# Optimization experiments

Measured on AMD Instinct MI355X. Metric: run time of the kernel, lower is better.

## Reference

```python
import jax, jax.numpy as jnp
import numpy as np

K = 3
PAD = 1
FS = 64  # feature_size == img_size for k=3, pad=1, stride=1
BN_EPS = 1e-5


def _unfold(x):
    # x: (B, C, H, W) -> (B, C*K*K, FS*FS), torch.nn.Unfold ordering (C-major, then kh, kw)
    B, C, H, W = x.shape
    xp = jnp.pad(x, ((0, 0), (0, 0), (PAD, PAD), (PAD, PAD)))
    patches = jnp.stack(
        [xp[:, :, i:i + FS, j:j + FS] for i in range(K) for j in range(K)],
        axis=2,
    )  # (B, C, K*K, FS, FS)
    return patches.reshape(B, C * K * K, FS * FS)


def setup_inputs() -> dict:
    key = jax.random.key(0)
    k1, k2, k3, k4, k5 = jax.random.split(key, 5)
    B, C, O = 32, 8, 32
    P = C * K * K  # 72
    return {
        "x": jax.random.normal(k1, (B, C, FS, FS), dtype=jnp.float32),
        "weight": jax.random.normal(k2, (1, O, P, FS * FS), dtype=jnp.float32) * 0.05,
        "bias": jax.random.normal(k3, (1, O, FS * FS), dtype=jnp.float32) * 0.05,
        "gamma": jax.random.uniform(k4, (O,), dtype=jnp.float32, minval=0.5, maxval=1.5),
        "beta": jax.random.normal(k5, (O,), dtype=jnp.float32) * 0.1,
    }


def reference(x, weight, bias, gamma, beta):
    B = x.shape[0]
    patches = _unfold(x)  # (B, P, F2)
    # per-pixel weights: (O, P, F2) contracted with patches over P
    y = jnp.einsum('opf,bpf->bof', weight[0], patches)  # (B, O, F2)
    y = y + bias  # (1, O, F2) broadcasts
    y = y.reshape(B, -1, FS, FS)
    # BatchNorm2d, training mode (biased batch variance)
    mean = jnp.mean(y, axis=(0, 2, 3), keepdims=True)
    var = jnp.mean(jnp.square(y - mean), axis=(0, 2, 3), keepdims=True)
    y = (y - mean) * jax.lax.rsqrt(var + BN_EPS)
    y = y * gamma[None, :, None, None] + beta[None, :, None, None]
    return y
```

## Files before the change

kernel.cpp:

```cpp
#include <hip/hip_runtime.h>

#define Oo    32
#define F2    4096
#define GRID  256
#define SLOTS 64
#define NTOT  (32 * F2)

typedef _Float16 h2 __attribute__((ext_vector_type(2)));
typedef _Float16 h8 __attribute__((ext_vector_type(8)));

#if __has_builtin(__builtin_amdgcn_fdot2)
#define DOT2(a, b, c) __builtin_amdgcn_fdot2((a), (b), (c), false)
#else
__device__ __forceinline__ float DOT2(h2 a, h2 b, float c) {
    return c + (float)a.x * (float)b.x + (float)a.y * (float)b.y;
}
#endif

__device__ __forceinline__ unsigned pkh2f(float a, float b) {
    h2 t; t.x = (_Float16)a; t.y = (_Float16)b;
    return __builtin_bit_cast(unsigned, t);
}
__device__ __forceinline__ h2 bch2(unsigned u) { return __builtin_bit_cast(h2, u); }

template <typename YT>
__global__ __launch_bounds__(512) void svconv_kernel(
    const float* __restrict__ x, const float* __restrict__ wgt,
    const float* __restrict__ bias, YT* __restrict__ y,
    float* __restrict__ psum, float* __restrict__ psumsq)
{
    __shared__ __align__(16) unsigned ldsX[3 * 32 * 68];
    __shared__ __align__(16) unsigned ldsW[2 * 9 * 8 * 64];

    const int tid = threadIdx.x;
    const int f   = tid & 63;
    const int bq  = tid >> 6;
    const int oq  = blockIdx.x >> 6;
    const int h   = blockIdx.x & 63;
    const int col = h * 64 + f;

    const bool wOK = (tid < 288);
    int wg = 0, wl = 0;
    {
        int s = wOK ? tid : 0;
        int o_ = s / 36, rm = s - 36 * o_;
        int k_ = rm >> 2, q_ = rm & 3;
        wg = ((oq * 8 + o_) * 72 + k_) * F2 + h * 64 + 16 * q_;
        wl = (k_ * 8 + o_) * 64 + 16 * q_;
    }

    bool xOK = false;
    int xg = 0, xl = 0;
    {
        int s = (tid < 384) ? tid : 0;
        int kh_ = s >> 7, b_ = (s >> 2) & 31, q_ = s & 3;
        int gh = h - 1 + kh_;
        xOK = (tid < 384) && ((unsigned)gh < 64u);
        xg = b_ * 32768 + gh * 64 + 16 * q_;
        xl = (kh_ * 32 + b_) * 68 + 16 * q_;
    }

    const int wi0 = (f == 0)  ? 64 : f - 1;
    const int wi2 = (f == 63) ? 65 : f + 1;

    float bz[8];
#pragma unroll
    for (int j = 0; j < 8; ++j) bz[j] = bias[(oq * 8 + j) * F2 + col];

    float acc[8][4];
#pragma unroll
    for (int j = 0; j < 8; ++j)
#pragma unroll
        for (int i = 0; i < 4; ++i) acc[j][i] = 0.f;

    float4 xr0[4], xr1[4], wr0[4], wr1[4];

    auto ISSUEX = [&](int cp) {
        if (xOK) {
            const int c0 = xg + cp * 8192;
#pragma unroll
            for (int e = 0; e < 4; ++e) {
                xr0[e] = *(const float4*)(x + c0 + 4 * e);
                xr1[e] = *(const float4*)(x + c0 + 4096 + 4 * e);
            }
        }
    };
    auto ISSUEW = [&](int cp) {
        if (wOK) {
            const int g0 = wg + cp * 18 * F2;
#pragma unroll
            for (int e = 0; e < 4; ++e) {
                wr0[e] = *(const float4*)(wgt + g0 + 4 * e);
                wr1[e] = *(const float4*)(wgt + g0 + 9 * F2 + 4 * e);
            }
        }
    };
    auto WRITEX = [&]() {
        if (xOK) {
#pragma unroll
            for (int e = 0; e < 4; ++e) {
                uint4 pk;
                pk.x = pkh2f(xr0[e].x, xr1[e].x);
                pk.y = pkh2f(xr0[e].y, xr1[e].y);
                pk.z = pkh2f(xr0[e].z, xr1[e].z);
                pk.w = pkh2f(xr0[e].w, xr1[e].w);
                *(uint4*)&ldsX[xl + 4 * e] = pk;
            }
        }
    };
    auto WRITEW = [&](int buf) {
        if (wOK) {
#pragma unroll
            for (int e = 0; e < 4; ++e) {
                uint4 pk;
                pk.x = pkh2f(wr0[e].x, wr1[e].x);
                pk.y = pkh2f(wr0[e].y, wr1[e].y);
                pk.z = pkh2f(wr0[e].z, wr1[e].z);
                pk.w = pkh2f(wr0[e].w, wr1[e].w);
                *(uint4*)&ldsW[buf * 4608 + wl + 4 * e] = pk;
            }
        }
    };
    auto COMPUTE = [&](int wbuf) {
        const unsigned* wb = &ldsW[wbuf * 4608];
#pragma unroll
        for (int k = 0; k < 9; ++k) {
            const int kh = k / 3, kw = k - 3 * kh;
            const int wi = (kw == 0) ? wi0 : ((kw == 1) ? f : wi2);
            h2 wv[8];
#pragma unroll
            for (int j = 0; j < 8; ++j) wv[j] = bch2(wb[k * 512 + j * 64 + f]);
#pragma unroll
            for (int i = 0; i < 4; ++i) {
                h2 xv = bch2(ldsX[(kh * 32 + bq * 4 + i) * 68 + wi]);
#pragma unroll
                for (int j = 0; j < 8; ++j)
                    acc[j][i] = DOT2(wv[j], xv, acc[j][i]);
            }
        }
    };

    ISSUEX(0); ISSUEW(0);
    for (int i = tid; i < 3 * 32 * 68; i += 512) ldsX[i] = 0u;
    __syncthreads();
    WRITEX(); WRITEW(0);
    ISSUEX(1); ISSUEW(1);
    __syncthreads();

#pragma unroll
    for (int cp = 0; cp < 4; ++cp) {
        COMPUTE(cp & 1);
        if (cp < 3) {
            __syncthreads();
            WRITEX(); WRITEW((cp + 1) & 1);
            if (cp < 2) { ISSUEX(cp + 2); ISSUEW(cp + 2); }
            __syncthreads();
        }
    }
    __syncthreads();

    float s_[8], ss_[8];
#pragma unroll
    for (int j = 0; j < 8; ++j) {
        s_[j] = 0.f; ss_[j] = 0.f;
#pragma unroll
        for (int i = 0; i < 4; ++i) {
            float a = acc[j][i] + bz[j];
            y[(size_t)((bq * 4 + i) * Oo + oq * 8 + j) * F2 + col] = (YT)a;
            s_[j] += a; ss_[j] = fmaf(a, a, ss_[j]);
        }
    }
    if (psum != nullptr) {
#pragma unroll
        for (int j = 0; j < 8; ++j)
#pragma unroll
            for (int d = 32; d >= 1; d >>= 1) {
                s_[j]  += __shfl_down(s_[j],  d, 64);
                ss_[j] += __shfl_down(ss_[j], d, 64);
            }
        float* scr = (float*)ldsX;
        if (f == 0) {
#pragma unroll
            for (int j = 0; j < 8; ++j) {
                scr[bq * 8 + j]      = s_[j];
                scr[64 + bq * 8 + j] = ss_[j];
            }
        }
        __syncthreads();
        if (tid < 64) {
            int j = tid >> 3, g = tid & 7;
            float v  = scr[g * 8 + j];
            float vv = scr[64 + g * 8 + j];
#pragma unroll
            for (int d = 4; d >= 1; d >>= 1) {
                v  += __shfl_down(v,  d, 8);
                vv += __shfl_down(vv, d, 8);
            }
            if (g == 0) {
                psum[(oq * 8 + j) * SLOTS + h]   = v;
                psumsq[(oq * 8 + j) * SLOTS + h] = vv;
            }
        }
    }
}

__global__ __launch_bounds__(64) void bnstats_kernel(
    const float* __restrict__ psum, const float* __restrict__ psumsq,
    const float* __restrict__ gamma, const float* __restrict__ beta,
    float* __restrict__ scsh)
{
    const int o = blockIdx.x;
    const int t = threadIdx.x;
    float s  = psum[o * SLOTS + t];
    float ss = psumsq[o * SLOTS + t];
#pragma unroll
    for (int d = 32; d >= 1; d >>= 1) {
        s  += __shfl_down(s, d, 64);
        ss += __shfl_down(ss, d, 64);
    }
    if (t == 0) {
        float mean = s / (float)NTOT;
        float var  = ss / (float)NTOT - mean * mean;
        float rstd = rsqrtf(var + 1e-5f);
        float scl  = gamma[o] * rstd;
        scsh[o]      = scl;
        scsh[Oo + o] = beta[o] - mean * scl;
    }
}

__global__ __launch_bounds__(256) void bnapply_f16_kernel(
    const _Float16* __restrict__ yh, const float* __restrict__ scsh,
    float* __restrict__ y)
{
    int i = blockIdx.x * 256 + threadIdx.x;
    h8 v = ((const h8*)yh)[i];
    int o = (i >> 9) & 31;
    float scl = scsh[o], sh = scsh[Oo + o];
    float4 lo, hi;
    lo.x = fmaf((float)v[0], scl, sh);
    lo.y = fmaf((float)v[1], scl, sh);
    lo.z = fmaf((float)v[2], scl, sh);
    lo.w = fmaf((float)v[3], scl, sh);
    hi.x = fmaf((float)v[4], scl, sh);
    hi.y = fmaf((float)v[5], scl, sh);
    hi.z = fmaf((float)v[6], scl, sh);
    hi.w = fmaf((float)v[7], scl, sh);
    ((float4*)y)[2 * i]     = lo;
    ((float4*)y)[2 * i + 1] = hi;
}

__global__ __launch_bounds__(256) void bnapply_kernel(
    float* __restrict__ y, const float* __restrict__ scsh)
{
    int i = blockIdx.x * 256 + threadIdx.x;
    float4 v = ((const float4*)y)[i];
    int o = (i >> 10) & 31;
    float scl = scsh[o], sh = scsh[Oo + o];
    v.x = fmaf(v.x, scl, sh);
    v.y = fmaf(v.y, scl, sh);
    v.z = fmaf(v.z, scl, sh);
    v.w = fmaf(v.w, scl, sh);
    ((float4*)y)[i] = v;
}

__global__ __launch_bounds__(256) void bnreduce_y_kernel(
    const float* __restrict__ y, float* __restrict__ seg, float* __restrict__ segsq)
{
    const int o  = blockIdx.x >> 3;
    const int sg = blockIdx.x & 7;
    const int t  = threadIdx.x;
    float s = 0.f, ss = 0.f;
    for (int i = t; i < 4 * 1024; i += 256) {
        int b   = sg * 4 + (i >> 10);
        int fof = (i & 1023) * 4;
        float4 v = *(const float4*)(y + (size_t)(b * Oo + o) * F2 + fof);
        s  += (v.x + v.y) + (v.z + v.w);
        ss += v.x * v.x + v.y * v.y + v.z * v.z + v.w * v.w;
    }
#pragma unroll
    for (int d = 32; d >= 1; d >>= 1) {
        s  += __shfl_down(s, d, 64);
        ss += __shfl_down(ss, d, 64);
    }
    __shared__ float ls[4], lss[4];
    int wv = t >> 6, ln = t & 63;
    if (ln == 0) { ls[wv] = s; lss[wv] = ss; }
    __syncthreads();
    if (t == 0) {
        seg[blockIdx.x]   = (ls[0] + ls[1]) + (ls[2] + ls[3]);
        segsq[blockIdx.x] = (lss[0] + lss[1]) + (lss[2] + lss[3]);
    }
}

__global__ __launch_bounds__(256) void bnstats2_kernel(
    const float* __restrict__ seg, const float* __restrict__ segsq,
    const float* __restrict__ gamma, const float* __restrict__ beta,
    float* __restrict__ scsh)
{
    const int t = threadIdx.x;
    const int o = t >> 3, g = t & 7;
    float v  = seg[t];
    float vv = segsq[t];
#pragma unroll
    for (int d = 4; d >= 1; d >>= 1) {
        v  += __shfl_down(v,  d, 8);
        vv += __shfl_down(vv, d, 8);
    }
    if (g == 0) {
        float mean = v / (float)NTOT;
        float var  = vv / (float)NTOT - mean * mean;
        float rstd = rsqrtf(var + 1e-5f);
        float scl  = gamma[o] * rstd;
        scsh[o]      = scl;
        scsh[Oo + o] = beta[o] - mean * scl;
    }
}

extern "C" void kernel_launch(void* const* d_in, const int* in_sizes, int n_in,
                              void* d_out, int out_size, void* d_ws, size_t ws_size,
                              hipStream_t stream)
{
    const float* x     = (const float*)d_in[0];
    const float* wgt   = (const float*)d_in[1];
    const float* bias  = (const float*)d_in[2];
    const float* gamma = (const float*)d_in[3];
    const float* beta  = (const float*)d_in[4];
    float* y = (float*)d_out;

    const size_t n_elems    = (size_t)NTOT * Oo;
    const size_t yh_bytes   = n_elems * sizeof(_Float16);
    const size_t psum_bytes = (size_t)(2 * Oo * SLOTS + 2 * Oo) * sizeof(float);

    if (ws_size >= yh_bytes + psum_bytes) {
        _Float16* yh  = (_Float16*)d_ws;
        float* psum   = (float*)((char*)d_ws + yh_bytes);
        float* psumsq = psum + Oo * SLOTS;
        float* scsh   = psumsq + Oo * SLOTS;
        svconv_kernel<_Float16><<<GRID, 512, 0, stream>>>(x, wgt, bias, yh, psum, psumsq);
        bnstats_kernel<<<Oo, 64, 0, stream>>>(psum, psumsq, gamma, beta, scsh);
        bnapply_f16_kernel<<<(int)(n_elems / 8 / 256), 256, 0, stream>>>(yh, scsh, y);
    } else if (ws_size >= psum_bytes) {
        float* psum   = (float*)d_ws;
        float* psumsq = psum + Oo * SLOTS;
        float* scsh   = psumsq + Oo * SLOTS;
        svconv_kernel<float><<<GRID, 512, 0, stream>>>(x, wgt, bias, y, psum, psumsq);
        bnstats_kernel<<<Oo, 64, 0, stream>>>(psum, psumsq, gamma, beta, scsh);
        bnapply_kernel<<<(int)(n_elems / 4 / 256), 256, 0, stream>>>(y, scsh);
    } else {
        float* seg   = (float*)d_ws;
        float* segsq = seg + 256;
        float* scsh  = segsq + 256;
        svconv_kernel<float><<<GRID, 512, 0, stream>>>(x, wgt, bias, y, nullptr, nullptr);
        bnreduce_y_kernel<<<256, 256, 0, stream>>>(y, seg, segsq);
        bnstats2_kernel<<<1, 256, 0, stream>>>(seg, segsq, gamma, beta, scsh);
        bnapply_kernel<<<(int)(n_elems / 4 / 256), 256, 0, stream>>>(y, scsh);
    }
}
```

Baseline: 32.06 us.

## Transpose LDS layouts for vector reads and double-buffer X with one barrier

Weights and inputs are stored in LDS in transposed, padded layouts: per-pixel weights are packed so the 8 output channels sit contiguously, and input is stored pixel-major with batch contiguous and halo columns. This lets COMPUTE fetch its operands with a few 128-bit LDS reads instead of many scalar reads per tap. X is now double-buffered like W, so each pipeline step writes the next buffer before computing the current one and needs one barrier instead of two. The trade-offs are scattered 32-bit LDS stores when writing X, strided global weight loads, and a larger LDS footprint.

```diff
diff --git a/kernel.cpp b/kernel.cpp
--- a/kernel.cpp
+++ b/kernel.cpp
@@ -5,6 +5,8 @@
 #define GRID  256
 #define SLOTS 64
 #define NTOT  (32 * F2)
+#define WBUF  6912
+#define XBUF  7128
 
 typedef _Float16 h2 __attribute__((ext_vector_type(2)));
 typedef _Float16 h8 __attribute__((ext_vector_type(8)));
@@ -29,8 +31,8 @@
     const float* __restrict__ bias, YT* __restrict__ y,
     float* __restrict__ psum, float* __restrict__ psumsq)
 {
-    __shared__ __align__(16) unsigned ldsX[3 * 32 * 68];
-    __shared__ __align__(16) unsigned ldsW[2 * 9 * 8 * 64];
+    __shared__ __align__(16) unsigned ldsW[2 * WBUF];
+    __shared__ __align__(16) unsigned ldsX[2 * XBUF];
 
     const int tid = threadIdx.x;
     const int f   = tid & 63;
@@ -43,25 +45,22 @@
     int wg = 0, wl = 0;
     {
         int s = wOK ? tid : 0;
-        int o_ = s / 36, rm = s - 36 * o_;
-        int k_ = rm >> 2, q_ = rm & 3;
-        wg = ((oq * 8 + o_) * 72 + k_) * F2 + h * 64 + 16 * q_;
-        wl = (k_ * 8 + o_) * 64 + 16 * q_;
+        int o4 = s / 144, rm = s - 144 * o4;
+        int k_ = rm >> 4, q_ = rm & 15;
+        wg = ((oq * 8 + o4 * 4) * 72 + k_) * F2 + h * 64 + 4 * q_;
+        wl = (k_ * 64 + 4 * q_) * 12 + o4 * 4;
     }
 
     bool xOK = false;
-    int xg = 0, xl = 0;
+    int xg = 0, xkh = 0, xq = 0, xb_ = 0;
     {
         int s = (tid < 384) ? tid : 0;
-        int kh_ = s >> 7, b_ = (s >> 2) & 31, q_ = s & 3;
-        int gh = h - 1 + kh_;
+        xkh = s >> 7; int r = s & 127;
+        xq = r >> 5; xb_ = r & 31;
+        int gh = h - 1 + xkh;
         xOK = (tid < 384) && ((unsigned)gh < 64u);
-        xg = b_ * 32768 + gh * 64 + 16 * q_;
-        xl = (kh_ * 32 + b_) * 68 + 16 * q_;
-    }
-
-    const int wi0 = (f == 0)  ? 64 : f - 1;
-    const int wi2 = (f == 63) ? 65 : f + 1;
+        xg = xb_ * 32768 + gh * 64 + 16 * xq;
+    }
 
     float bz[8];
 #pragma unroll
@@ -73,7 +72,7 @@
 #pragma unroll
         for (int i = 0; i < 4; ++i) acc[j][i] = 0.f;
 
-    float4 xr0[4], xr1[4], wr0[4], wr1[4];
+    float4 xr0[4], xr1[4], wA[4], wB[4];
 
     auto ISSUEX = [&](int cp) {
         if (xOK) {
@@ -89,75 +88,73 @@
         if (wOK) {
             const int g0 = wg + cp * 18 * F2;
 #pragma unroll
+            for (int j = 0; j < 4; ++j) {
+                wA[j] = *(const float4*)(wgt + g0 + j * 72 * F2);
+                wB[j] = *(const float4*)(wgt + g0 + j * 72 * F2 + 9 * F2);
+            }
+        }
+    };
+    auto WRITEX = [&](int buf) {
+        if (xOK) {
+            unsigned* xd = ldsX + buf * XBUF + xkh * (66 * 36) + xb_;
+#pragma unroll
             for (int e = 0; e < 4; ++e) {
-                wr0[e] = *(const float4*)(wgt + g0 + 4 * e);
-                wr1[e] = *(const float4*)(wgt + g0 + 9 * F2 + 4 * e);
-            }
-        }
-    };
-    auto WRITEX = [&]() {
-        if (xOK) {
-#pragma unroll
-            for (int e = 0; e < 4; ++e) {
-                uint4 pk;
-                pk.x = pkh2f(xr0[e].x, xr1[e].x);
-                pk.y = pkh2f(xr0[e].y, xr1[e].y);
-                pk.z = pkh2f(xr0[e].z, xr1[e].z);
-                pk.w = pkh2f(xr0[e].w, xr1[e].w);
-                *(uint4*)&ldsX[xl + 4 * e] = pk;
+                const float* a = (const float*)&xr0[e];
+                const float* b = (const float*)&xr1[e];
+#pragma unroll
+                for (int i = 0; i < 4; ++i)
+                    xd[(16 * xq + 4 * e + i + 1) * 36] = pkh2f(a[i], b[i]);
             }
         }
     };
     auto WRITEW = [&](int buf) {
         if (wOK) {
-#pragma unroll
-            for (int e = 0; e < 4; ++e) {
+            unsigned* wd = ldsW + buf * WBUF + wl;
+#pragma unroll
+            for (int i = 0; i < 4; ++i) {
                 uint4 pk;
-                pk.x = pkh2f(wr0[e].x, wr1[e].x);
-                pk.y = pkh2f(wr0[e].y, wr1[e].y);
-                pk.z = pkh2f(wr0[e].z, wr1[e].z);
-                pk.w = pkh2f(wr0[e].w, wr1[e].w);
-                *(uint4*)&ldsW[buf * 4608 + wl + 4 * e] = pk;
-            }
-        }
-    };
-    auto COMPUTE = [&](int wbuf) {
-        const unsigned* wb = &ldsW[wbuf * 4608];
+                pk.x = pkh2f(((const float*)&wA[0])[i], ((const float*)&wB[0])[i]);
+                pk.y = pkh2f(((const float*)&wA[1])[i], ((const float*)&wB[1])[i]);
+                pk.z = pkh2f(((const float*)&wA[2])[i], ((const float*)&wB[2])[i]);
+                pk.w = pkh2f(((const float*)&wA[3])[i], ((const float*)&wB[3])[i]);
+                *(uint4*)(wd + i * 12) = pk;
+            }
+        }
+    };
+    auto COMPUTE = [&](int buf) {
+        const unsigned* wb = ldsW + buf * WBUF;
+        const unsigned* xb = ldsX + buf * XBUF;
 #pragma unroll
         for (int k = 0; k < 9; ++k) {
             const int kh = k / 3, kw = k - 3 * kh;
-            const int wi = (kw == 0) ? wi0 : ((kw == 1) ? f : wi2);
-            h2 wv[8];
-#pragma unroll
-            for (int j = 0; j < 8; ++j) wv[j] = bch2(wb[k * 512 + j * 64 + f]);
-#pragma unroll
-            for (int i = 0; i < 4; ++i) {
-                h2 xv = bch2(ldsX[(kh * 32 + bq * 4 + i) * 68 + wi]);
-#pragma unroll
-                for (int j = 0; j < 8; ++j)
-                    acc[j][i] = DOT2(wv[j], xv, acc[j][i]);
-            }
+            uint4 wlo = *(const uint4*)(wb + (k * 64 + f) * 12);
+            uint4 whi = *(const uint4*)(wb + (k * 64 + f) * 12 + 4);
+            uint4 xu  = *(const uint4*)(xb + (kh * 66 + f + kw) * 36 + bq * 4);
+            h2 wv[8] = { bch2(wlo.x), bch2(wlo.y), bch2(wlo.z), bch2(wlo.w),
+                         bch2(whi.x), bch2(whi.y), bch2(whi.z), bch2(whi.w) };
+            h2 xv[4] = { bch2(xu.x), bch2(xu.y), bch2(xu.z), bch2(xu.w) };
+#pragma unroll
+            for (int j = 0; j < 8; ++j)
+#pragma unroll
+                for (int i = 0; i < 4; ++i)
+                    acc[j][i] = DOT2(wv[j], xv[i], acc[j][i]);
         }
     };
 
     ISSUEX(0); ISSUEW(0);
-    for (int i = tid; i < 3 * 32 * 68; i += 512) ldsX[i] = 0u;
+    for (int i = tid; i < 2 * XBUF; i += 512) ldsX[i] = 0u;
     __syncthreads();
-    WRITEX(); WRITEW(0);
+    WRITEX(0); WRITEW(0);
     ISSUEX(1); ISSUEW(1);
     __syncthreads();
 
 #pragma unroll
     for (int cp = 0; cp < 4; ++cp) {
+        if (cp < 3) { WRITEX((cp + 1) & 1); WRITEW((cp + 1) & 1); }
+        if (cp < 2) { ISSUEX(cp + 2); ISSUEW(cp + 2); }
         COMPUTE(cp & 1);
-        if (cp < 3) {
-            __syncthreads();
-            WRITEX(); WRITEW((cp + 1) & 1);
-            if (cp < 2) { ISSUEX(cp + 2); ISSUEW(cp + 2); }
-            __syncthreads();
-        }
-    }
-    __syncthreads();
+        __syncthreads();
+    }
 
     float s_[8], ss_[8];
 #pragma unroll
```

Result: slower. 34.53 us (+7.7%).

## Fuse conv, BN statistics and BN apply via cooperative grid sync

Applied to the files above, without the earlier changes.

Replaces the three-kernel path (conv writing fp16 intermediate, stats kernel, apply kernel) with a single cooperative kernel. Each block keeps its accumulators in registers, publishes per-block partial sums, waits on a grid-wide barrier, reduces the statistics for its eight channels and writes the normalized output directly. This removes the intermediate write and re-read plus two launches. In exchange it adds a grid sync, and the 256 blocks of 512 threads must all be co-resident.

```diff
diff --git a/kernel.cpp b/kernel.cpp
--- a/kernel.cpp
+++ b/kernel.cpp
@@ -1,4 +1,7 @@
 #include <hip/hip_runtime.h>
+#include <hip/hip_cooperative_groups.h>
+
+namespace cg = cooperative_groups;
 
 #define Oo    32
 #define F2    4096
@@ -7,7 +10,6 @@
 #define NTOT  (32 * F2)
 
 typedef _Float16 h2 __attribute__((ext_vector_type(2)));
-typedef _Float16 h8 __attribute__((ext_vector_type(8)));
 
 #if __has_builtin(__builtin_amdgcn_fdot2)
 #define DOT2(a, b, c) __builtin_amdgcn_fdot2((a), (b), (c), false)
@@ -23,14 +25,15 @@
 }
 __device__ __forceinline__ h2 bch2(unsigned u) { return __builtin_bit_cast(h2, u); }
 
-template <typename YT>
-__global__ __launch_bounds__(512) void svconv_kernel(
+__global__ __launch_bounds__(512) void svconv_fused(
     const float* __restrict__ x, const float* __restrict__ wgt,
-    const float* __restrict__ bias, YT* __restrict__ y,
+    const float* __restrict__ bias, const float* __restrict__ gamma,
+    const float* __restrict__ beta, float* __restrict__ y,
     float* __restrict__ psum, float* __restrict__ psumsq)
 {
     __shared__ __align__(16) unsigned ldsX[3 * 32 * 68];
     __shared__ __align__(16) unsigned ldsW[2 * 9 * 8 * 64];
+    __shared__ float scls[8], shfs[8];
 
     const int tid = threadIdx.x;
     const int f   = tid & 63;
@@ -166,18 +169,18 @@
 #pragma unroll
         for (int i = 0; i < 4; ++i) {
             float a = acc[j][i] + bz[j];
-            y[(size_t)((bq * 4 + i) * Oo + oq * 8 + j) * F2 + col] = (YT)a;
+            acc[j][i] = a;
             s_[j] += a; ss_[j] = fmaf(a, a, ss_[j]);
         }
     }
-    if (psum != nullptr) {
-#pragma unroll
-        for (int j = 0; j < 8; ++j)
-#pragma unroll
-            for (int d = 32; d >= 1; d >>= 1) {
-                s_[j]  += __shfl_down(s_[j],  d, 64);
-                ss_[j] += __shfl_down(ss_[j], d, 64);
-            }
+#pragma unroll
+    for (int j = 0; j < 8; ++j)
+#pragma unroll
+        for (int d = 32; d >= 1; d >>= 1) {
+            s_[j]  += __shfl_down(s_[j],  d, 64);
+            ss_[j] += __shfl_down(ss_[j], d, 64);
+        }
+    {
         float* scr = (float*)ldsX;
         if (f == 0) {
 #pragma unroll
@@ -202,65 +205,175 @@
             }
         }
     }
-}
-
-__global__ __launch_bounds__(64) void bnstats_kernel(
-    const float* __restrict__ psum, const float* __restrict__ psumsq,
-    const float* __restrict__ gamma, const float* __restrict__ beta,
-    float* __restrict__ scsh)
-{
-    const int o = blockIdx.x;
-    const int t = threadIdx.x;
-    float s  = psum[o * SLOTS + t];
-    float ss = psumsq[o * SLOTS + t];
-#pragma unroll
-    for (int d = 32; d >= 1; d >>= 1) {
-        s  += __shfl_down(s, d, 64);
-        ss += __shfl_down(ss, d, 64);
-    }
-    if (t == 0) {
-        float mean = s / (float)NTOT;
-        float var  = ss / (float)NTOT - mean * mean;
-        float rstd = rsqrtf(var + 1e-5f);
-        float scl  = gamma[o] * rstd;
-        scsh[o]      = scl;
-        scsh[Oo + o] = beta[o] - mean * scl;
-    }
-}
-
-__global__ __launch_bounds__(256) void bnapply_f16_kernel(
-    const _Float16* __restrict__ yh, const float* __restrict__ scsh,
-    float* __restrict__ y)
-{
-    int i = blockIdx.x * 256 + threadIdx.x;
-    h8 v = ((const h8*)yh)[i];
-    int o = (i >> 9) & 31;
-    float scl = scsh[o], sh = scsh[Oo + o];
-    float4 lo, hi;
-    lo.x = fmaf((float)v[0], scl, sh);
-    lo.y = fmaf((float)v[1], scl, sh);
-    lo.z = fmaf((float)v[2], scl, sh);
-    lo.w = fmaf((float)v[3], scl, sh);
-    hi.x = fmaf((float)v[4], scl, sh);
-    hi.y = fmaf((float)v[5], scl, sh);
-    hi.z = fmaf((float)v[6], scl, sh);
-    hi.w = fmaf((float)v[7], scl, sh);
-    ((float4*)y)[2 * i]     = lo;
-    ((float4*)y)[2 * i + 1] = hi;
-}
-
-__global__ __launch_bounds__(256) void bnapply_kernel(
-    float* __restrict__ y, const float* __restrict__ scsh)
-{
-    int i = blockIdx.x * 256 + threadIdx.x;
-    float4 v = ((const float4*)y)[i];
-    int o = (i >> 10) & 31;
-    float scl = scsh[o], sh = scsh[Oo + o];
-    v.x = fmaf(v.x, scl, sh);
-    v.y = fmaf(v.y, scl, sh);
-    v.z = fmaf(v.z, scl, sh);
-    v.w = fmaf(v.w, scl, sh);
-    ((float4*)y)[i] = v;
+
+    __threadfence();
+    cg::this_grid().sync();
+
+    {
+        const int j8 = tid >> 6;
+        const int sl = tid & 63;
+        const int o  = oq * 8 + j8;
+        float v  = psum[o * SLOTS + sl];
+        float vv = psumsq[o * SLOTS + sl];
+#pragma unroll
+        for (int d = 32; d >= 1; d >>= 1) {
+            v  += __shfl_down(v,  d, 64);
+            vv += __shfl_down(vv, d, 64);
+        }
+        if (sl == 0) {
+            float mean = v / (float)NTOT;
+            float var  = vv / (float)NTOT - mean * mean;
+            float rstd = rsqrtf(var + 1e-5f);
+            float scl  = gamma[o] * rstd;
+            scls[j8] = scl;
+            shfs[j8] = beta[o] - mean * scl;
+        }
+    }
+    __syncthreads();
+
+#pragma unroll
+    for (int j = 0; j < 8; ++j) {
+        const float scl = scls[j], sh = shfs[j];
+#pragma unroll
+        for (int i = 0; i < 4; ++i) {
+            y[(size_t)((bq * 4 + i) * Oo + oq * 8 + j) * F2 + col] =
+                fmaf(acc[j][i], scl, sh);
+        }
+    }
+}
+
+__global__ __launch_bounds__(512) void svconv_plain(
+    const float* __restrict__ x, const float* __restrict__ wgt,
+    const float* __restrict__ bias, float* __restrict__ y)
+{
+    __shared__ __align__(16) unsigned ldsX[3 * 32 * 68];
+    __shared__ __align__(16) unsigned ldsW[2 * 9 * 8 * 64];
+
+    const int tid = threadIdx.x;
+    const int f   = tid & 63;
+    const int bq  = tid >> 6;
+    const int oq  = blockIdx.x >> 6;
+    const int h   = blockIdx.x & 63;
+    const int col = h * 64 + f;
+
+    const bool wOK = (tid < 288);
+    int wg = 0, wl = 0;
+    {
+        int s = wOK ? tid : 0;
+        int o_ = s / 36, rm = s - 36 * o_;
+        int k_ = rm >> 2, q_ = rm & 3;
+        wg = ((oq * 8 + o_) * 72 + k_) * F2 + h * 64 + 16 * q_;
+        wl = (k_ * 8 + o_) * 64 + 16 * q_;
+    }
+    bool xOK = false;
+    int xg = 0, xl = 0;
+    {
+        int s = (tid < 384) ? tid : 0;
+        int kh_ = s >> 7, b_ = (s >> 2) & 31, q_ = s & 3;
+        int gh = h - 1 + kh_;
+        xOK = (tid < 384) && ((unsigned)gh < 64u);
+        xg = b_ * 32768 + gh * 64 + 16 * q_;
+        xl = (kh_ * 32 + b_) * 68 + 16 * q_;
+    }
+    const int wi0 = (f == 0)  ? 64 : f - 1;
+    const int wi2 = (f == 63) ? 65 : f + 1;
+
+    float bz[8];
+#pragma unroll
+    for (int j = 0; j < 8; ++j) bz[j] = bias[(oq * 8 + j) * F2 + col];
+    float acc[8][4];
+#pragma unroll
+    for (int j = 0; j < 8; ++j)
+#pragma unroll
+        for (int i = 0; i < 4; ++i) acc[j][i] = 0.f;
+
+    float4 xr0[4], xr1[4], wr0[4], wr1[4];
+    auto ISSUEX = [&](int cp) {
+        if (xOK) {
+            const int c0 = xg + cp * 8192;
+#pragma unroll
+            for (int e = 0; e < 4; ++e) {
+                xr0[e] = *(const float4*)(x + c0 + 4 * e);
+                xr1[e] = *(const float4*)(x + c0 + 4096 + 4 * e);
+            }
+        }
+    };
+    auto ISSUEW = [&](int cp) {
+        if (wOK) {
+            const int g0 = wg + cp * 18 * F2;
+#pragma unroll
+            for (int e = 0; e < 4; ++e) {
+                wr0[e] = *(const float4*)(wgt + g0 + 4 * e);
+                wr1[e] = *(const float4*)(wgt + g0 + 9 * F2 + 4 * e);
+            }
+        }
+    };
+    auto WRITEX = [&]() {
+        if (xOK) {
+#pragma unroll
+            for (int e = 0; e < 4; ++e) {
+                uint4 pk;
+                pk.x = pkh2f(xr0[e].x, xr1[e].x);
+                pk.y = pkh2f(xr0[e].y, xr1[e].y);
+                pk.z = pkh2f(xr0[e].z, xr1[e].z);
+                pk.w = pkh2f(xr0[e].w, xr1[e].w);
+                *(uint4*)&ldsX[xl + 4 * e] = pk;
+            }
+        }
+    };
+    auto WRITEW = [&](int buf) {
+        if (wOK) {
+#pragma unroll
+            for (int e = 0; e < 4; ++e) {
+                uint4 pk;
+                pk.x = pkh2f(wr0[e].x, wr1[e].x);
+                pk.y = pkh2f(wr0[e].y, wr1[e].y);
+                pk.z = pkh2f(wr0[e].z, wr1[e].z);
+                pk.w = pkh2f(wr0[e].w, wr1[e].w);
+                *(uint4*)&ldsW[buf * 4608 + wl + 4 * e] = pk;
+            }
+        }
+    };
+    auto COMPUTE = [&](int wbuf) {
+        const unsigned* wb = &ldsW[wbuf * 4608];
+#pragma unroll
+        for (int k = 0; k < 9; ++k) {
+            const int kh = k / 3, kw = k - 3 * kh;
+            const int wi = (kw == 0) ? wi0 : ((kw == 1) ? f : wi2);
+            h2 wv[8];
+#pragma unroll
+            for (int j = 0; j < 8; ++j) wv[j] = bch2(wb[k * 512 + j * 64 + f]);
+#pragma unroll
+            for (int i = 0; i < 4; ++i) {
+                h2 xv = bch2(ldsX[(kh * 32 + bq * 4 + i) * 68 + wi]);
+#pragma unroll
+                for (int j = 0; j < 8; ++j)
+                    acc[j][i] = DOT2(wv[j], xv, acc[j][i]);
+            }
+        }
+    };
+
+    ISSUEX(0); ISSUEW(0);
+    for (int i = tid; i < 3 * 32 * 68; i += 512) ldsX[i] = 0u;
+    __syncthreads();
+    WRITEX(); WRITEW(0);
+    ISSUEX(1); ISSUEW(1);
+    __syncthreads();
+#pragma unroll
+    for (int cp = 0; cp < 4; ++cp) {
+        COMPUTE(cp & 1);
+        if (cp < 3) {
+            __syncthreads();
+            WRITEX(); WRITEW((cp + 1) & 1);
+            if (cp < 2) { ISSUEX(cp + 2); ISSUEW(cp + 2); }
+            __syncthreads();
+        }
+    }
+#pragma unroll
+    for (int j = 0; j < 8; ++j)
+#pragma unroll
+        for (int i = 0; i < 4; ++i)
+            y[(size_t)((bq * 4 + i) * Oo + oq * 8 + j) * F2 + col] = acc[j][i] + bz[j];
 }
 
 __global__ __launch_bounds__(256) void bnreduce_y_kernel(
@@ -316,6 +429,20 @@
     }
 }
 
+__global__ __launch_bounds__(256) void bnapply_kernel(
+    float* __restrict__ y, const float* __restrict__ scsh)
+{
+    int i = blockIdx.x * 256 + threadIdx.x;
+    float4 v = ((const float4*)y)[i];
+    int o = (i >> 10) & 31;
+    float scl = scsh[o], sh = scsh[Oo + o];
+    v.x = fmaf(v.x, scl, sh);
+    v.y = fmaf(v.y, scl, sh);
+    v.z = fmaf(v.z, scl, sh);
+    v.w = fmaf(v.w, scl, sh);
+    ((float4*)y)[i] = v;
+}
+
 extern "C" void kernel_launch(void* const* d_in, const int* in_sizes, int n_in,
                               void* d_out, int out_size, void* d_ws, size_t ws_size,
                               hipStream_t stream)
@@ -328,29 +455,20 @@
     float* y = (float*)d_out;
 
     const size_t n_elems    = (size_t)NTOT * Oo;
-    const size_t yh_bytes   = n_elems * sizeof(_Float16);
-    const size_t psum_bytes = (size_t)(2 * Oo * SLOTS + 2 * Oo) * sizeof(float);
-
-    if (ws_size >= yh_bytes + psum_bytes) {
-        _Float16* yh  = (_Float16*)d_ws;
-        float* psum   = (float*)((char*)d_ws + yh_bytes);
-        float* psumsq = psum + Oo * SLOTS;
-        float* scsh   = psumsq + Oo * SLOTS;
-        svconv_kernel<_Float16><<<GRID, 512, 0, stream>>>(x, wgt, bias, yh, psum, psumsq);
-        bnstats_kernel<<<Oo, 64, 0, stream>>>(psum, psumsq, gamma, beta, scsh);
-        bnapply_f16_kernel<<<(int)(n_elems / 8 / 256), 256, 0, stream>>>(yh, scsh, y);
-    } else if (ws_size >= psum_bytes) {
+    const size_t psum_bytes = (size_t)(2 * Oo * SLOTS) * sizeof(float);
+
+    if (ws_size >= psum_bytes) {
         float* psum   = (float*)d_ws;
         float* psumsq = psum + Oo * SLOTS;
-        float* scsh   = psumsq + Oo * SLOTS;
-        svconv_kernel<float><<<GRID, 512, 0, stream>>>(x, wgt, bias, y, psum, psumsq);
-        bnstats_kernel<<<Oo, 64, 0, stream>>>(psum, psumsq, gamma, beta, scsh);
-        bnapply_kernel<<<(int)(n_elems / 4 / 256), 256, 0, stream>>>(y, scsh);
+        void* args[] = { (void*)&x, (void*)&wgt, (void*)&bias, (void*)&gamma,
+                         (void*)&beta, (void*)&y, (void*)&psum, (void*)&psumsq };
+        hipLaunchCooperativeKernel((void*)svconv_fused, dim3(GRID), dim3(512),
+                                   args, 0, stream);
     } else {
         float* seg   = (float*)d_ws;
         float* segsq = seg + 256;
         float* scsh  = segsq + 256;
-        svconv_kernel<float><<<GRID, 512, 0, stream>>>(x, wgt, bias, y, nullptr, nullptr);
+        svconv_plain<<<GRID, 512, 0, stream>>>(x, wgt, bias, y);
         bnreduce_y_kernel<<<256, 256, 0, stream>>>(y, seg, segsq);
         bnstats2_kernel<<<1, 256, 0, stream>>>(seg, segsq, gamma, beta, scsh);
         bnapply_kernel<<<(int)(n_elems / 4 / 256), 256, 0, stream>>>(y, scsh);
```

After: 87.73 us. +173.6%, slower.
